# Kernel tuning notes

Measured on AMD Instinct MI355X. Metric: run time of the kernel, lower is better.

## Reference

```python
import jax, jax.numpy as jnp
import numpy as np


def setup_inputs() -> dict:
    key = jax.random.key(0)
    k_u, k_a, k_b, k_c, k_d = jax.random.split(key, 5)
    B, T, Din, Dout, S = 16, 4096, 256, 256, 256
    return {
        "u": jax.random.normal(k_u, (B, T, Din), dtype=jnp.float32),
        "a_raw": jnp.zeros((S,), dtype=jnp.float32),
        "b": jax.random.normal(k_b, (S, Din), dtype=jnp.float32) * 0.1,
        "c": jax.random.normal(k_c, (Dout, S), dtype=jnp.float32) * 0.1,
        "d": jax.random.normal(k_d, (Dout, Din), dtype=jnp.float32) * 0.1,
    }


def reference(u, a_raw, b, c, d):
    # u: (B, T, Din) -> y: (B, T, Dout)
    # Recurrence: x_t = a * x_{t-1} + b @ u_t ;  y_t = c @ x_t + d @ u_t
    a = jnp.tanh(a_raw)                                  # (S,)
    Bu = jnp.einsum('btd,sd->bts', u, b)                 # input projection, (B,T,S)

    def step(x, bu_t):
        x = x * a + bu_t                                 # diagonal state update
        return x, x

    x0 = jnp.zeros((u.shape[0], a.shape[0]), dtype=u.dtype)
    _, xs = jax.lax.scan(step, x0, jnp.swapaxes(Bu, 0, 1))  # xs: (T,B,S)
    xs = jnp.swapaxes(xs, 0, 1)                              # (B,T,S)

    y = jnp.einsum('bts,os->bto', xs, c) + jnp.einsum('bti,oi->bto', u, d)
    return y  # dropout(p=0.0) is identity
```

## Files before the change

kernel.cpp:

```cpp
#include <hip/hip_runtime.h>

#define DEV __device__ __forceinline__

typedef unsigned short u16;
typedef __attribute__((ext_vector_type(8))) __bf16 bf16x8;
typedef __attribute__((ext_vector_type(4))) float f32x4;
typedef __attribute__((ext_vector_type(8))) unsigned short u16x8;
typedef __attribute__((ext_vector_type(4))) unsigned short u16x4;

static constexpr int NB = 16;
static constexpr int NT = 4096;
static constexpr int NCH = 64;
static constexpr int LCH = 64;

DEV u16 f2bf(float f) {
  unsigned u = __builtin_bit_cast(unsigned, f);
  u += 0x7fffu + ((u >> 16) & 1u);
  return (u16)(u >> 16);
}
DEV float bf2f(u16 h) {
  unsigned u = ((unsigned)h) << 16;
  return __builtin_bit_cast(float, u);
}

DEV void gl_lds16(const void* gp, void* lp) {
  __builtin_amdgcn_global_load_lds(
      (__attribute__((address_space(1))) void*)(void*)gp,
      (__attribute__((address_space(3))) void*)lp, 16, 0, 0);
}

DEV u16x8 pack8(float4 a, float4 b) {
  u16x8 o;
  o[0] = f2bf(a.x); o[1] = f2bf(a.y); o[2] = f2bf(a.z); o[3] = f2bf(a.w);
  o[4] = f2bf(b.x); o[5] = f2bf(b.y); o[6] = f2bf(b.z); o[7] = f2bf(b.w);
  return o;
}

__global__ __launch_bounds__(256) void prep_k(const float* __restrict__ a_raw,
                                              const float* __restrict__ b,
                                              const float* __restrict__ c,
                                              const float* __restrict__ d,
                                              float* __restrict__ af,
                                              u16* __restrict__ bw,
                                              u16* __restrict__ cw,
                                              u16* __restrict__ dw) {
  int i = blockIdx.x * 256 + threadIdx.x;
  if (i < 256) af[i] = tanhf(a_raw[i]);
  bw[i] = f2bf(b[i]);
  cw[i] = f2bf(c[i]);
  dw[i] = f2bf(d[i]);
}

__global__ __launch_bounds__(512) void gemm1_k(const float* __restrict__ u,
                                               const u16* __restrict__ bw,
                                               const u16* __restrict__ dw,
                                               u16* __restrict__ bu,
                                               u16* __restrict__ ud) {
  __shared__ u16 As[128 * 64];
  __shared__ u16 Bs[128 * 64];
  const int tid = threadIdx.x;
  const int lane = tid & 63;
  const int wid = tid >> 6;
  const int wr = wid >> 2, wc = wid & 3;
  const int bx = blockIdx.x;
  const int by = blockIdx.y;
  const bool dpanel = (by >= 2);
  const int col0 = (by & 1) * 128;
  const u16* W = dpanel ? dw : bw;
  const size_t row0 = (size_t)bx * 128;

  const int arow = tid >> 2;
  const int ak0 = (tid & 3) * 16;
  const float* uptr = u + (row0 + arow) * 256;
  const int s0 = (tid & 3) * 2;

  const f32x4 zero = {0.f, 0.f, 0.f, 0.f};
  f32x4 acc[4][2];
#pragma unroll
  for (int i = 0; i < 4; ++i) { acc[i][0] = zero; acc[i][1] = zero; }

#pragma unroll
  for (int kt = 0; kt < 4; ++kt) {
    const int kb = kt * 64;
    float4 f0 = *reinterpret_cast<const float4*>(uptr + kb + ak0);
    float4 f1 = *reinterpret_cast<const float4*>(uptr + kb + ak0 + 4);
    float4 f2 = *reinterpret_cast<const float4*>(uptr + kb + ak0 + 8);
    float4 f3 = *reinterpret_cast<const float4*>(uptr + kb + ak0 + 12);
#pragma unroll
    for (int r = 0; r < 2; ++r) {
      int brow = r * 64 + (tid >> 3);
      int sc = (tid & 7) ^ (brow & 7);
      gl_lds16(W + (size_t)(col0 + brow) * 256 + kb + sc * 8,
               (char*)Bs + r * 8192 + wid * 1024);
    }
    *reinterpret_cast<u16x8*>(&As[arow * 64 + ((s0) ^ (arow & 7)) * 8]) = pack8(f0, f1);
    *reinterpret_cast<u16x8*>(&As[arow * 64 + ((s0 + 1) ^ (arow & 7)) * 8]) = pack8(f2, f3);
    __syncthreads();
#pragma unroll
    for (int kk = 0; kk < 2; ++kk) {
      const int ks = kk * 4 + (lane >> 4);
      bf16x8 afr[4], bfr[2];
#pragma unroll
      for (int mi = 0; mi < 4; ++mi) {
        int ar = wr * 64 + mi * 16 + (lane & 15);
        afr[mi] = *reinterpret_cast<const bf16x8*>(&As[ar * 64 + (ks ^ (ar & 7)) * 8]);
      }
#pragma unroll
      for (int ni = 0; ni < 2; ++ni) {
        int nr = wc * 32 + ni * 16 + (lane & 15);
        bfr[ni] = *reinterpret_cast<const bf16x8*>(&Bs[nr * 64 + (ks ^ (nr & 7)) * 8]);
      }
#pragma unroll
      for (int mi = 0; mi < 4; ++mi)
#pragma unroll
        for (int ni = 0; ni < 2; ++ni)
          acc[mi][ni] = __builtin_amdgcn_mfma_f32_16x16x32_bf16(
              afr[mi], bfr[ni], acc[mi][ni], 0, 0, 0);
    }
    if (kt < 3) __syncthreads();
  }

#pragma unroll
  for (int mi = 0; mi < 4; ++mi) {
    int rlb = wr * 64 + mi * 16 + (lane >> 4) * 4;
#pragma unroll
    for (int ni = 0; ni < 2; ++ni) {
      int col = col0 + wc * 32 + ni * 16 + (lane & 15);
#pragma unroll
      for (int q = 0; q < 4; ++q) {
        size_t R = row0 + rlb + q;
        u16 h = f2bf(acc[mi][ni][q]);
        if (!dpanel)
          bu[R * 256 + (((col >> 3) ^ ((int)(R) & 7)) * 8) + (col & 7)] = h;
        else
          ud[R * 256 + col] = h;
      }
    }
  }
}

__global__ __launch_bounds__(256) void scan1_k(const u16* __restrict__ bu,
                                               const float* __restrict__ af,
                                               float* __restrict__ carry) {
  const int tid = threadIdx.x;
  const int g = blockIdx.x * 4 + (tid >> 6);
  const int s4 = (tid & 63) * 4;
  const size_t rb = (size_t)g * 64;
  float a0 = af[s4], a1 = af[s4 + 1], a2 = af[s4 + 2], a3 = af[s4 + 3];
  float x0 = 0.f, x1 = 0.f, x2 = 0.f, x3 = 0.f;
  for (int t = 0; t < LCH; ++t) {
    size_t idx = (rb + t) * 256 + ((s4 >> 3) ^ (t & 7)) * 8 + (s4 & 7);
    u16x4 v = *reinterpret_cast<const u16x4*>(bu + idx);
    x0 = fmaf(a0, x0, bf2f(v[0]));
    x1 = fmaf(a1, x1, bf2f(v[1]));
    x2 = fmaf(a2, x2, bf2f(v[2]));
    x3 = fmaf(a3, x3, bf2f(v[3]));
  }
  float4 o = {x0, x1, x2, x3};
  *reinterpret_cast<float4*>(carry + (size_t)g * 256 + s4) = o;
}

__global__ __launch_bounds__(256) void scan2_k(const float* __restrict__ carry,
                                               const float* __restrict__ af,
                                               float* __restrict__ initb) {
  int b = blockIdx.x;
  int s = threadIdx.x;
  float a = af[s];
  float aL = a;
#pragma unroll
  for (int i = 0; i < 6; ++i) aL *= aL;
  float x = 0.f;
  for (int k = 0; k < NCH; ++k) {
    size_t idx = ((size_t)(b * NCH + k)) * 256 + s;
    float cv = carry[idx];
    initb[idx] = x;
    x = fmaf(aL, x, cv);
  }
}

__global__ __launch_bounds__(512) void gemm2_k(const u16* __restrict__ bu,
                                               const u16* __restrict__ cw,
                                               const u16* __restrict__ ud,
                                               const float* __restrict__ af,
                                               const float* __restrict__ initb,
                                               float* __restrict__ y) {
  __shared__ u16 XS[128 * 256];
  __shared__ u16 CS[128 * 64];
  const int tid = threadIdx.x;
  const int lane = tid & 63;
  const int wid = tid >> 6;
  const int wr = wid >> 2, wc = wid & 3;
  const int bx = blockIdx.x;
  const int col0 = blockIdx.y * 128;

  const char* src = (const char*)bu + (size_t)bx * 65536;
#pragma unroll
  for (int j = 0; j < 8; ++j)
    gl_lds16(src + j * 8192 + tid * 16, (char*)XS + j * 8192 + wid * 1024);
#pragma unroll
  for (int r = 0; r < 2; ++r) {
    int brow = r * 64 + (tid >> 3);
    int sc = (tid & 7) ^ (brow & 7);
    gl_lds16(cw + (size_t)(col0 + brow) * 256 + 0 + sc * 8,
             (char*)CS + r * 8192 + wid * 1024);
  }
  __syncthreads();

  {
    const int hf = tid >> 8;
    const int s = tid & 255;
    const float a = af[s];
    float x = initb[(size_t)(bx * 2 + hf) * 256 + s];
    const int r0 = hf * 64;
    const int slot = s >> 3;
    const int off = (s & 7);
#pragma unroll 8
    for (int t = 0; t < 64; ++t) {
      int r = r0 + t;
      int bi = r * 256 + ((slot ^ (r & 7)) * 8) + off;
      x = fmaf(a, x, bf2f(XS[bi]));
      XS[bi] = f2bf(x);
    }
  }

  f32x4 acc[4][2];
#pragma unroll
  for (int mi = 0; mi < 4; ++mi) {
    int rlb = wr * 64 + mi * 16 + (lane >> 4) * 4;
#pragma unroll
    for (int ni = 0; ni < 2; ++ni) {
      int col = col0 + wc * 32 + ni * 16 + (lane & 15);
#pragma unroll
      for (int q = 0; q < 4; ++q)
        acc[mi][ni][q] = bf2f(ud[(size_t)(bx * 128 + rlb + q) * 256 + col]);
    }
  }
  __syncthreads();

#pragma unroll
  for (int kt = 0; kt < 4; ++kt) {
#pragma unroll
    for (int kk = 0; kk < 2; ++kk) {
      const int ksl = kk * 4 + (lane >> 4);
      const int ksg = kt * 8 + ksl;
      bf16x8 afr[4], bfr[2];
#pragma unroll
      for (int mi = 0; mi < 4; ++mi) {
        int ar = wr * 64 + mi * 16 + (lane & 15);
        afr[mi] = *reinterpret_cast<const bf16x8*>(&XS[ar * 256 + ((ksg ^ (ar & 7)) * 8)]);
      }
#pragma unroll
      for (int ni = 0; ni < 2; ++ni) {
        int nr = wc * 32 + ni * 16 + (lane & 15);
        bfr[ni] = *reinterpret_cast<const bf16x8*>(&CS[nr * 64 + ((ksl ^ (nr & 7)) * 8)]);
      }
#pragma unroll
      for (int mi = 0; mi < 4; ++mi)
#pragma unroll
        for (int ni = 0; ni < 2; ++ni)
          acc[mi][ni] = __builtin_amdgcn_mfma_f32_16x16x32_bf16(
              afr[mi], bfr[ni], acc[mi][ni], 0, 0, 0);
    }
    if (kt < 3) {
      __syncthreads();
#pragma unroll
      for (int r = 0; r < 2; ++r) {
        int brow = r * 64 + (tid >> 3);
        int sc = (tid & 7) ^ (brow & 7);
        gl_lds16(cw + (size_t)(col0 + brow) * 256 + (kt + 1) * 64 + sc * 8,
                 (char*)CS + r * 8192 + wid * 1024);
      }
      __syncthreads();
    }
  }

#pragma unroll
  for (int mi = 0; mi < 4; ++mi) {
    int rlb = wr * 64 + mi * 16 + (lane >> 4) * 4;
#pragma unroll
    for (int ni = 0; ni < 2; ++ni) {
      int col = col0 + wc * 32 + ni * 16 + (lane & 15);
#pragma unroll
      for (int q = 0; q < 4; ++q)
        y[(size_t)(bx * 128 + rlb + q) * 256 + col] = acc[mi][ni][q];
    }
  }
}

extern "C" void kernel_launch(void* const* d_in, const int* in_sizes, int n_in,
                              void* d_out, int out_size, void* d_ws, size_t ws_size,
                              hipStream_t stream) {
  const float* u = (const float*)d_in[0];
  const float* a_raw = (const float*)d_in[1];
  const float* b = (const float*)d_in[2];
  const float* c = (const float*)d_in[3];
  const float* d = (const float*)d_in[4];
  float* y = (float*)d_out;
  char* ws = (char*)d_ws;

  const size_t MB = 1u << 20;
  float* af = (float*)(ws);
  u16* bw = (u16*)(ws + 4096);
  u16* cw = (u16*)(ws + 4096 + 131072);
  u16* dw = (u16*)(ws + 4096 + 2 * 131072);
  u16* bu = (u16*)(ws + 1 * MB);
  u16* ud = (u16*)(ws + 33 * MB);
  float* carry = (float*)(ws + 65 * MB);
  float* initb = (float*)(ws + 66 * MB);

  prep_k<<<256, 256, 0, stream>>>(a_raw, b, c, d, af, bw, cw, dw);
  gemm1_k<<<dim3(512, 4), 512, 0, stream>>>(u, bw, dw, bu, ud);
  scan1_k<<<256, 256, 0, stream>>>(bu, af, carry);
  scan2_k<<<16, 256, 0, stream>>>(carry, af, initb);
  gemm2_k<<<dim3(512, 2), 512, 0, stream>>>(bu, cw, ud, af, initb, y);
}
```

Before: 107.3 us.

## Fuse chunk-carry scan into input GEMM and compute full N=512 per block

The b and d weights are concatenated into one 512-row matrix, so each gemm1 block computes a 64-row tile against both projections. Each u tile is then read and converted once instead of four times. The per-chunk carry reduction is computed from the fp32 accumulators with powers of a and a cross-lane shuffle reduction, which removes the separate scan1 kernel and its re-read of bu. In exchange, blocks use 1024 threads and 72KB of LDS, which lowers occupancy, and the carry now comes from unrounded fp32 values rather than the bf16-rounded bu.

Result: faster. 91.53 us (-14.7%).

```diff
diff --git a/kernel.cpp b/kernel.cpp
--- a/kernel.cpp
+++ b/kernel.cpp
@@ -29,50 +29,37 @@
       (__attribute__((address_space(3))) void*)lp, 16, 0, 0);
 }
 
-DEV u16x8 pack8(float4 a, float4 b) {
-  u16x8 o;
-  o[0] = f2bf(a.x); o[1] = f2bf(a.y); o[2] = f2bf(a.z); o[3] = f2bf(a.w);
-  o[4] = f2bf(b.x); o[5] = f2bf(b.y); o[6] = f2bf(b.z); o[7] = f2bf(b.w);
-  return o;
-}
-
 __global__ __launch_bounds__(256) void prep_k(const float* __restrict__ a_raw,
                                               const float* __restrict__ b,
                                               const float* __restrict__ c,
                                               const float* __restrict__ d,
                                               float* __restrict__ af,
-                                              u16* __restrict__ bw,
-                                              u16* __restrict__ cw,
-                                              u16* __restrict__ dw) {
+                                              u16* __restrict__ wq,
+                                              u16* __restrict__ cw) {
   int i = blockIdx.x * 256 + threadIdx.x;
   if (i < 256) af[i] = tanhf(a_raw[i]);
-  bw[i] = f2bf(b[i]);
+  wq[i] = f2bf(b[i]);
+  wq[65536 + i] = f2bf(d[i]);
   cw[i] = f2bf(c[i]);
-  dw[i] = f2bf(d[i]);
-}
-
-__global__ __launch_bounds__(512) void gemm1_k(const float* __restrict__ u,
-                                               const u16* __restrict__ bw,
-                                               const u16* __restrict__ dw,
-                                               u16* __restrict__ bu,
-                                               u16* __restrict__ ud) {
-  __shared__ u16 As[128 * 64];
-  __shared__ u16 Bs[128 * 64];
+}
+
+__global__ __launch_bounds__(1024) void gemm1_k(const float* __restrict__ u,
+                                                const u16* __restrict__ wq,
+                                                const float* __restrict__ af,
+                                                u16* __restrict__ bu,
+                                                u16* __restrict__ ud,
+                                                float* __restrict__ carry) {
+  __shared__ u16 As[64 * 64];
+  __shared__ u16 Ws[512 * 64];
   const int tid = threadIdx.x;
   const int lane = tid & 63;
   const int wid = tid >> 6;
-  const int wr = wid >> 2, wc = wid & 3;
   const int bx = blockIdx.x;
-  const int by = blockIdx.y;
-  const bool dpanel = (by >= 2);
-  const int col0 = (by & 1) * 128;
-  const u16* W = dpanel ? dw : bw;
-  const size_t row0 = (size_t)bx * 128;
-
-  const int arow = tid >> 2;
-  const int ak0 = (tid & 3) * 16;
-  const float* uptr = u + (row0 + arow) * 256;
-  const int s0 = (tid & 3) * 2;
+  const size_t row0 = (size_t)bx * 64;
+
+  const int arow = tid >> 4;
+  const int ak = (tid & 15) * 4;
+  const int abyte = arow * 128 + ((((tid & 15) >> 1) ^ (arow & 7)) * 16) + (tid & 1) * 8;
 
   const f32x4 zero = {0.f, 0.f, 0.f, 0.f};
   f32x4 acc[4][2];
@@ -82,19 +69,17 @@
 #pragma unroll
   for (int kt = 0; kt < 4; ++kt) {
     const int kb = kt * 64;
-    float4 f0 = *reinterpret_cast<const float4*>(uptr + kb + ak0);
-    float4 f1 = *reinterpret_cast<const float4*>(uptr + kb + ak0 + 4);
-    float4 f2 = *reinterpret_cast<const float4*>(uptr + kb + ak0 + 8);
-    float4 f3 = *reinterpret_cast<const float4*>(uptr + kb + ak0 + 12);
-#pragma unroll
-    for (int r = 0; r < 2; ++r) {
-      int brow = r * 64 + (tid >> 3);
-      int sc = (tid & 7) ^ (brow & 7);
-      gl_lds16(W + (size_t)(col0 + brow) * 256 + kb + sc * 8,
-               (char*)Bs + r * 8192 + wid * 1024);
-    }
-    *reinterpret_cast<u16x8*>(&As[arow * 64 + ((s0) ^ (arow & 7)) * 8]) = pack8(f0, f1);
-    *reinterpret_cast<u16x8*>(&As[arow * 64 + ((s0 + 1) ^ (arow & 7)) * 8]) = pack8(f2, f3);
+    float4 av = *reinterpret_cast<const float4*>(u + (row0 + arow) * 256 + kb + ak);
+#pragma unroll
+    for (int r = 0; r < 4; ++r) {
+      int wrow = r * 128 + (tid >> 3);
+      int sc = (tid & 7) ^ (wrow & 7);
+      gl_lds16(wq + (size_t)wrow * 256 + kb + sc * 8,
+               (char*)Ws + r * 16384 + wid * 1024);
+    }
+    u16x4 a4;
+    a4[0] = f2bf(av.x); a4[1] = f2bf(av.y); a4[2] = f2bf(av.z); a4[3] = f2bf(av.w);
+    *reinterpret_cast<u16x4*>((char*)As + abyte) = a4;
     __syncthreads();
 #pragma unroll
     for (int kk = 0; kk < 2; ++kk) {
@@ -102,13 +87,15 @@
       bf16x8 afr[4], bfr[2];
 #pragma unroll
       for (int mi = 0; mi < 4; ++mi) {
-        int ar = wr * 64 + mi * 16 + (lane & 15);
-        afr[mi] = *reinterpret_cast<const bf16x8*>(&As[ar * 64 + (ks ^ (ar & 7)) * 8]);
+        int ar = mi * 16 + (lane & 15);
+        afr[mi] = *reinterpret_cast<const bf16x8*>(
+            (const char*)As + ar * 128 + ((ks ^ (ar & 7)) * 16));
       }
 #pragma unroll
       for (int ni = 0; ni < 2; ++ni) {
-        int nr = wc * 32 + ni * 16 + (lane & 15);
-        bfr[ni] = *reinterpret_cast<const bf16x8*>(&Bs[nr * 64 + (ks ^ (nr & 7)) * 8]);
+        int br = wid * 32 + ni * 16 + (lane & 15);
+        bfr[ni] = *reinterpret_cast<const bf16x8*>(
+            (const char*)Ws + br * 128 + ((ks ^ (br & 7)) * 16));
       }
 #pragma unroll
       for (int mi = 0; mi < 4; ++mi)
@@ -122,42 +109,47 @@
 
 #pragma unroll
   for (int mi = 0; mi < 4; ++mi) {
-    int rlb = wr * 64 + mi * 16 + (lane >> 4) * 4;
+    int rl = mi * 16 + (lane >> 4) * 4;
 #pragma unroll
     for (int ni = 0; ni < 2; ++ni) {
-      int col = col0 + wc * 32 + ni * 16 + (lane & 15);
+      int col = wid * 32 + ni * 16 + (lane & 15);
 #pragma unroll
       for (int q = 0; q < 4; ++q) {
-        size_t R = row0 + rlb + q;
+        size_t R = row0 + rl + q;
         u16 h = f2bf(acc[mi][ni][q]);
-        if (!dpanel)
-          bu[R * 256 + (((col >> 3) ^ ((int)(R) & 7)) * 8) + (col & 7)] = h;
+        if (wid < 8)
+          bu[R * 256 + (((col >> 3) ^ ((int)R & 7)) * 8) + (col & 7)] = h;
         else
-          ud[R * 256 + col] = h;
-      }
-    }
-  }
-}
-
-__global__ __launch_bounds__(256) void scan1_k(const u16* __restrict__ bu,
-                                               const float* __restrict__ af,
-                                               float* __restrict__ carry) {
-  const int tid = threadIdx.x;
-  const int g = blockIdx.x * 4 + (tid >> 6);
-  const int s4 = (tid & 63) * 4;
-  const size_t rb = (size_t)g * 64;
-  float a0 = af[s4], a1 = af[s4 + 1], a2 = af[s4 + 2], a3 = af[s4 + 3];
-  float x0 = 0.f, x1 = 0.f, x2 = 0.f, x3 = 0.f;
-  for (int t = 0; t < LCH; ++t) {
-    size_t idx = (rb + t) * 256 + ((s4 >> 3) ^ (t & 7)) * 8 + (s4 & 7);
-    u16x4 v = *reinterpret_cast<const u16x4*>(bu + idx);
-    x0 = fmaf(a0, x0, bf2f(v[0]));
-    x1 = fmaf(a1, x1, bf2f(v[1]));
-    x2 = fmaf(a2, x2, bf2f(v[2]));
-    x3 = fmaf(a3, x3, bf2f(v[3]));
-  }
-  float4 o = {x0, x1, x2, x3};
-  *reinterpret_cast<float4*>(carry + (size_t)g * 256 + s4) = o;
+          ud[R * 256 + (col - 256)] = h;
+      }
+    }
+  }
+
+  if (wid < 8) {
+    const int tb = (lane >> 4) * 4;
+#pragma unroll
+    for (int ni = 0; ni < 2; ++ni) {
+      int col = wid * 32 + ni * 16 + (lane & 15);
+      float a = af[col];
+      float c2 = a * a, c4 = c2 * c2, c8 = c4 * c4;
+      float a12 = c8 * c4;
+      float a13 = a12 * a;
+      float base = (tb == 0) ? a12 : (tb == 4) ? c8 : (tb == 8) ? c4 : 1.0f;
+      float p = base, s = 0.f;
+#pragma unroll
+      for (int mi = 3; mi >= 0; --mi) {
+#pragma unroll
+        for (int q = 3; q >= 0; --q) {
+          s = fmaf(p, acc[mi][ni][q], s);
+          if (q) p *= a;
+        }
+        if (mi) p *= a13;
+      }
+      s += __shfl_xor(s, 16, 64);
+      s += __shfl_xor(s, 32, 64);
+      if ((lane >> 4) == 0) carry[(size_t)bx * 256 + col] = s;
+    }
+  }
 }
 
 __global__ __launch_bounds__(256) void scan2_k(const float* __restrict__ carry,
@@ -300,17 +292,15 @@
 
   const size_t MB = 1u << 20;
   float* af = (float*)(ws);
-  u16* bw = (u16*)(ws + 4096);
-  u16* cw = (u16*)(ws + 4096 + 131072);
-  u16* dw = (u16*)(ws + 4096 + 2 * 131072);
+  u16* wq = (u16*)(ws + 65536);
+  u16* cw = (u16*)(ws + 65536 + 262144);
   u16* bu = (u16*)(ws + 1 * MB);
   u16* ud = (u16*)(ws + 33 * MB);
   float* carry = (float*)(ws + 65 * MB);
   float* initb = (float*)(ws + 66 * MB);
 
-  prep_k<<<256, 256, 0, stream>>>(a_raw, b, c, d, af, bw, cw, dw);
-  gemm1_k<<<dim3(512, 4), 512, 0, stream>>>(u, bw, dw, bu, ud);
-  scan1_k<<<256, 256, 0, stream>>>(bu, af, carry);
+  prep_k<<<256, 256, 0, stream>>>(a_raw, b, c, d, af, wq, cw);
+  gemm1_k<<<1024, 1024, 0, stream>>>(u, wq, af, bu, ud, carry);
   scan2_k<<<16, 256, 0, stream>>>(carry, af, initb);
   gemm2_k<<<dim3(512, 2), 512, 0, stream>>>(bu, cw, ud, af, initb, y);
 }
```
